# Optimization experiments

Hardware: AMD Instinct MI355X
Metric: run time of the kernel (lower is better)

The kernel has to match this reference:

```python
import jax, jax.numpy as jnp
import numpy as np

NUM_HEADS = 16
WIN_H, WIN_W = 7, 7
DIM = 512
N = WIN_H * WIN_W  # 49 tokens per window
B_ = 2048          # num_windows * batch
NUM_WINDOWS = 64


def _relative_pos_indices(win_h, win_w):
    ch, cw = np.meshgrid(np.arange(win_h), np.arange(win_w), indexing='ij')
    coords = np.stack([ch, cw], axis=-1).reshape(-1, 2)          # (N, 2)
    rel = coords[None, :, :] - coords[:, None, :]                # (N, N, 2)
    rel[:, :, 0] += win_h - 1
    rel[:, :, 1] += win_w - 1
    rel[:, :, 0] *= 2 * win_w - 1
    return rel.sum(-1).reshape(-1).astype(np.int32)             # (N*N,)


def setup_inputs() -> dict:
    key = jax.random.key(0)
    k1, k2, k3, k4, k5 = jax.random.split(key, 5)
    x = jax.random.normal(k1, (B_, N, DIM), dtype=jnp.float32)
    # 0 / -100 shift mask (finite stand-in for -inf; same softmax effect)
    u = jax.random.uniform(k2, (NUM_WINDOWS, N, N))
    mask = jnp.where(u < 0.2, -100.0, 0.0).astype(jnp.float32)
    qkv_w = jax.random.normal(k3, (DIM, 3 * DIM), dtype=jnp.float32) * 0.02
    qkv_b = jnp.zeros((3 * DIM,), jnp.float32)
    proj_w = jax.random.normal(k4, (DIM, DIM), dtype=jnp.float32) * 0.02
    proj_b = jnp.zeros((DIM,), jnp.float32)
    bias_table = jax.random.normal(k5, ((2 * WIN_H - 1) * (2 * WIN_W - 1), NUM_HEADS), dtype=jnp.float32) * 0.02
    rel_idx = jnp.asarray(_relative_pos_indices(WIN_H, WIN_W))
    return {"x": x, "mask": mask, "qkv_w": qkv_w, "qkv_b": qkv_b,
            "proj_w": proj_w, "proj_b": proj_b,
            "bias_table": bias_table, "rel_idx": rel_idx}


def reference(x, mask, qkv_w, qkv_b, proj_w, proj_b, bias_table, rel_idx):
    b_, n, c = x.shape
    h = NUM_HEADS
    d = c // h
    scale = d ** -0.5
    qkv = (x @ qkv_w + qkv_b).reshape(b_, n, 3, h, d)
    q, k, v = jnp.moveaxis(qkv, 2, 0)                 # each (b_, n, h, d)
    attn = jnp.einsum('bnhd,bmhd->bhnm', q * scale, k)  # (b_, h, n, n)
    # relative-position bias gather: (n*n,) -> (n, n, h) -> (h, n, n)
    bias = bias_table[rel_idx].reshape(n, n, h).transpose(2, 0, 1)
    attn = attn + bias[None]
    nw = mask.shape[0]
    attn = attn.reshape(b_ // nw, nw, h, n, n) + mask[None, :, None]
    attn = jax.nn.softmax(attn.reshape(b_, h, n, n), axis=-1)
    out = jnp.einsum('bhnm,bmhd->bnhd', attn, v).reshape(b_, n, c)
    return out @ proj_w + proj_b
```

## Files before the change

kernel.cpp:

```cpp
#include <hip/hip_runtime.h>
#include <stdint.h>

typedef __attribute__((ext_vector_type(8))) short short8;
typedef __attribute__((ext_vector_type(8))) unsigned short ushort8;
typedef __attribute__((ext_vector_type(4))) unsigned short bf16x4;
typedef __attribute__((ext_vector_type(4))) float float4_t;

#define AS1 __attribute__((address_space(1)))
#define AS3 __attribute__((address_space(3)))

__device__ __forceinline__ unsigned short f2bf(float f) {
    union { float f; unsigned u; } c; c.f = f;
    return (unsigned short)((c.u + 0x7fffu + ((c.u >> 16) & 1u)) >> 16);
}

__device__ __forceinline__ void load16_lds(const void* g, void* l) {
    __builtin_amdgcn_global_load_lds((const AS1 void*)(uintptr_t)g,
                                     (AS3 void*)(uintptr_t)l, 16, 0, 0);
}

__global__ __launch_bounds__(256)
void cvt_x(const float4_t* __restrict__ x, unsigned short* __restrict__ xb, int n8) {
    int i = blockIdx.x * 256 + threadIdx.x;
    if (i >= n8) return;
    float4_t a = x[2 * i], b = x[2 * i + 1];
    ushort8 v;
    v[0] = f2bf(a[0]); v[1] = f2bf(a[1]); v[2] = f2bf(a[2]); v[3] = f2bf(a[3]);
    v[4] = f2bf(b[0]); v[5] = f2bf(b[1]); v[6] = f2bf(b[2]); v[7] = f2bf(b[3]);
    ((ushort8*)xb)[i] = v;
}

__global__ __launch_bounds__(256)
void prep(const float* __restrict__ qkv_w, const float* __restrict__ proj_w,
          const float* __restrict__ bias_tab, const int* __restrict__ rel_idx,
          const float* __restrict__ mask,
          unsigned short* __restrict__ qkv_wT, unsigned short* __restrict__ proj_wT,
          float* __restrict__ biasP, float* __restrict__ maskP) {
    int i = blockIdx.x * 256 + threadIdx.x;
    if (i < 786432) {
        int n = i >> 9, k = i & 511;
        qkv_wT[i] = f2bf(qkv_w[k * 1536 + n]);
    } else if (i < 1048576) {
        int j = i - 786432;
        int n = j >> 9, k = j & 511;
        proj_wT[j] = f2bf(proj_w[k * 512 + n]);
    } else if (i < 1098752) {
        int j = i - 1048576;
        int h = j / 3136, mn = j % 3136;
        int m = mn >> 6, n = mn & 63;
        biasP[j] = (n < 49) ? bias_tab[rel_idx[m * 49 + n] * 16 + h] : 0.0f;
    } else {
        int j = i - 1098752;
        int w = j / 3136, mn = j % 3136;
        int m = mn >> 6, n = mn & 63;
        maskP[j] = (n < 49) ? mask[w * 2401 + m * 49 + n] : -1e30f;
    }
}

template <int MODE>
__global__ __launch_bounds__(256)
void gemm_bt(const unsigned short* __restrict__ A, const unsigned short* __restrict__ B,
             void* __restrict__ Cv, const float* __restrict__ bias,
             int M, int N, int K, float qscale) {
    __shared__ __align__(16) unsigned short As[4 * 128 * 32];
    __shared__ __align__(16) unsigned short Bs[4 * 128 * 32];

    const int t = threadIdx.x;
    const int lane = t & 63;
    const int wave = t >> 6;
    const int col = lane & 15;
    const int quad = lane >> 4;
    const int wm = (wave & 1) * 64;
    const int wn = (wave >> 1) * 64;

    const int nwg = gridDim.x;
    const int cpx = nwg >> 3;
    const int wg = (blockIdx.x & 7) * cpx + (blockIdx.x >> 3);
    const int nbx = N >> 7;
    const int m0 = (wg / nbx) * 128;
    const int n0 = (wg % nbx) * 128;

    float4_t acc[4][4] = {};

    const int row = t >> 2;
    const int seg = t & 3;
    const unsigned short* Ag0 = A + (size_t)(m0 + row) * K + seg * 8;
    const unsigned short* Ag1 = A + (size_t)(m0 + 64 + row) * K + seg * 8;
    const unsigned short* Bg0 = B + (size_t)(n0 + row) * K + seg * 8;
    const unsigned short* Bg1 = B + (size_t)(n0 + 64 + row) * K + seg * 8;

    auto stage = [&](int tile) {
        const int kk = tile << 5;
        unsigned short* Ad = As + ((tile & 3) << 12);
        unsigned short* Bd = Bs + ((tile & 3) << 12);
        load16_lds(Ag0 + kk, Ad + t * 8);
        load16_lds(Ag1 + kk, Ad + 2048 + t * 8);
        load16_lds(Bg0 + kk, Bd + t * 8);
        load16_lds(Bg1 + kk, Bd + 2048 + t * 8);
    };

    const int nt = K >> 5;
    stage(0); stage(1); stage(2);

    for (int tt = 0; tt < nt; ++tt) {
        if (tt < nt - 2)       asm volatile("s_waitcnt vmcnt(8)" ::: "memory");
        else if (tt == nt - 2) asm volatile("s_waitcnt vmcnt(4)" ::: "memory");
        else                   asm volatile("s_waitcnt vmcnt(0)" ::: "memory");
        __builtin_amdgcn_s_barrier();
        asm volatile("" ::: "memory");

        if (tt + 3 < nt) stage(tt + 3);

        const unsigned short* Ab = As + ((size_t)(tt & 3) << 12);
        const unsigned short* Bb = Bs + ((size_t)(tt & 3) << 12);
        short8 a[4], b[4];
#pragma unroll
        for (int i = 0; i < 4; ++i)
            a[i] = *(const short8*)&Ab[(wm + i * 16 + col) * 32 + quad * 8];
#pragma unroll
        for (int j = 0; j < 4; ++j)
            b[j] = *(const short8*)&Bb[(wn + j * 16 + col) * 32 + quad * 8];
        __builtin_amdgcn_s_setprio(1);
#pragma unroll
        for (int i = 0; i < 4; ++i)
#pragma unroll
            for (int j = 0; j < 4; ++j)
                acc[i][j] = __builtin_amdgcn_mfma_f32_16x16x32_bf16(b[j], a[i], acc[i][j], 0, 0, 0);
        __builtin_amdgcn_s_setprio(0);
    }

    if (MODE == 0) {
        unsigned short* C = (unsigned short*)Cv;
#pragma unroll
        for (int j = 0; j < 4; ++j) {
            int gc0 = n0 + wn + j * 16 + quad * 4;
            float4_t bv = *(const float4_t*)&bias[gc0];
            float sc = (gc0 < 512) ? qscale : 1.0f;
#pragma unroll
            for (int i = 0; i < 4; ++i) {
                int gr = m0 + wm + i * 16 + col;
                bf16x4 u;
#pragma unroll
                for (int r = 0; r < 4; ++r) u[r] = f2bf((acc[i][j][r] + bv[r]) * sc);
                *(bf16x4*)&C[(size_t)gr * N + gc0] = u;
            }
        }
    } else {
        float* C = (float*)Cv;
#pragma unroll
        for (int j = 0; j < 4; ++j) {
            int gc0 = n0 + wn + j * 16 + quad * 4;
            float4_t bv = *(const float4_t*)&bias[gc0];
#pragma unroll
            for (int i = 0; i < 4; ++i) {
                int gr = m0 + wm + i * 16 + col;
                float4_t ov = acc[i][j] + bv;
                *(float4_t*)&C[(size_t)gr * N + gc0] = ov;
            }
        }
    }
}

__global__ __launch_bounds__(64)
void attn_win(const unsigned short* __restrict__ qkv,
              const float* __restrict__ maskP,
              const float* __restrict__ biasP,
              unsigned short* __restrict__ attn_out) {
    __shared__ __align__(16) unsigned short P[64 * 64];
    __shared__ __align__(16) unsigned short Vt[32 * 64];

    const int bh = blockIdx.x;
    const int w = bh >> 4;
    const int hh = bh & 15;
    const int lane = threadIdx.x;
    const int col = lane & 15;
    const int quad = lane >> 4;
    const size_t rowbase = (size_t)(w * 49) * 1536;

    {
        ushort8 u0 = {}, u1 = {}, u2 = {}, u3 = {};
        if (lane < 49) {
            const ushort8* vp = (const ushort8*)(qkv + rowbase + (size_t)lane * 1536 + 1024 + hh * 32);
            u0 = vp[0]; u1 = vp[1]; u2 = vp[2]; u3 = vp[3];
        }
#pragma unroll
        for (int c = 0; c < 8; ++c) {
            Vt[((c) * 64 + lane) ^ ((c & 7) << 3)] = u0[c];
            Vt[((c + 8) * 64 + lane) ^ ((c & 7) << 3)] = u1[c];
            Vt[((c + 16) * 64 + lane) ^ ((c & 7) << 3)] = u2[c];
            Vt[((c + 24) * 64 + lane) ^ ((c & 7) << 3)] = u3[c];
        }
    }

    float4_t s[4][4] = {};
    {
        short8 qf[4], kf[4];
#pragma unroll
        for (int i = 0; i < 4; ++i) {
            int m = i * 16 + col; if (m > 48) m = 48;
            qf[i] = *(const short8*)(qkv + rowbase + (size_t)m * 1536 + hh * 32 + quad * 8);
            kf[i] = *(const short8*)(qkv + rowbase + (size_t)m * 1536 + 512 + hh * 32 + quad * 8);
        }
        __builtin_amdgcn_s_setprio(1);
#pragma unroll
        for (int i = 0; i < 4; ++i)
#pragma unroll
            for (int j = 0; j < 4; ++j)
                s[i][j] = __builtin_amdgcn_mfma_f32_16x16x32_bf16(kf[j], qf[i], s[i][j], 0, 0, 0);
        __builtin_amdgcn_s_setprio(0);
    }

    {
        const float* mk = maskP + (size_t)(w & 63) * 3136;
        const float* bs = biasP + (size_t)hh * 3136;
#pragma unroll
        for (int i = 0; i < 4; ++i) {
            int mc = i * 16 + col; if (mc > 48) mc = 48;
#pragma unroll
            for (int j = 0; j < 4; ++j) {
                int n0 = j * 16 + quad * 4;
                float4_t a4 = *(const float4_t*)&mk[mc * 64 + n0];
                float4_t b4 = *(const float4_t*)&bs[mc * 64 + n0];
#pragma unroll
                for (int r = 0; r < 4; ++r) s[i][j][r] += a4[r] + b4[r];
            }
        }
    }

#pragma unroll
    for (int i = 0; i < 4; ++i) {
        int m = i * 16 + col;
        float mx = s[i][0][0];
#pragma unroll
        for (int j = 0; j < 4; ++j)
#pragma unroll
            for (int r = 0; r < 4; ++r) mx = fmaxf(mx, s[i][j][r]);
        mx = fmaxf(mx, __shfl_xor(mx, 16));
        mx = fmaxf(mx, __shfl_xor(mx, 32));
        float sum = 0.f;
#pragma unroll
        for (int j = 0; j < 4; ++j)
#pragma unroll
            for (int r = 0; r < 4; ++r) {
                float e = __expf(s[i][j][r] - mx);
                s[i][j][r] = e; sum += e;
            }
        sum += __shfl_xor(sum, 16);
        sum += __shfl_xor(sum, 32);
        float inv = 1.0f / sum;
#pragma unroll
        for (int j = 0; j < 4; ++j) {
            bf16x4 u;
#pragma unroll
            for (int r = 0; r < 4; ++r) u[r] = f2bf(s[i][j][r] * inv);
            *(bf16x4*)&P[(m * 64 + j * 16 + quad * 4) ^ ((m & 7) << 3)] = u;
        }
    }
    __syncthreads();

    float4_t o[4][2] = {};
#pragma unroll
    for (int s2 = 0; s2 < 2; ++s2) {
        short8 pa[4], vb[2];
#pragma unroll
        for (int i = 0; i < 4; ++i) {
            int m = i * 16 + col;
            pa[i] = *(const short8*)&P[(m * 64 + s2 * 32 + quad * 8) ^ ((m & 7) << 3)];
        }
#pragma unroll
        for (int tj = 0; tj < 2; ++tj) {
            int d = tj * 16 + col;
            vb[tj] = *(const short8*)&Vt[(d * 64 + s2 * 32 + quad * 8) ^ ((d & 7) << 3)];
        }
        __builtin_amdgcn_s_setprio(1);
#pragma unroll
        for (int i = 0; i < 4; ++i)
#pragma unroll
            for (int tj = 0; tj < 2; ++tj)
                o[i][tj] = __builtin_amdgcn_mfma_f32_16x16x32_bf16(vb[tj], pa[i], o[i][tj], 0, 0, 0);
        __builtin_amdgcn_s_setprio(0);
    }

#pragma unroll
    for (int i = 0; i < 4; ++i) {
        int m = i * 16 + col;
        if (m < 49) {
            size_t ob = (size_t)(w * 49 + m) * 512 + hh * 32 + quad * 4;
#pragma unroll
            for (int tj = 0; tj < 2; ++tj) {
                bf16x4 u;
#pragma unroll
                for (int r = 0; r < 4; ++r) u[r] = f2bf(o[i][tj][r]);
                *(bf16x4*)&attn_out[ob + tj * 16] = u;
            }
        }
    }
}

extern "C" void kernel_launch(void* const* d_in, const int* in_sizes, int n_in,
                              void* d_out, int out_size, void* d_ws, size_t ws_size,
                              hipStream_t stream) {
    const float* x        = (const float*)d_in[0];
    const float* mask     = (const float*)d_in[1];
    const float* qkv_w    = (const float*)d_in[2];
    const float* qkv_b    = (const float*)d_in[3];
    const float* proj_w   = (const float*)d_in[4];
    const float* proj_b   = (const float*)d_in[5];
    const float* bias_tab = (const float*)d_in[6];
    const int*   rel_idx  = (const int*)d_in[7];
    float* out = (float*)d_out;

    char* ws = (char*)d_ws;
    size_t off = 0;
    auto carve = [&](size_t bytes) -> char* {
        char* p = ws + off;
        off += (bytes + 255) & ~(size_t)255;
        return p;
    };
    unsigned short* x_bf    = (unsigned short*)carve((size_t)51380224 * 2);
    unsigned short* qkv_wT  = (unsigned short*)carve((size_t)786432 * 2);
    unsigned short* proj_wT = (unsigned short*)carve((size_t)262144 * 2);
    float*          biasP   = (float*)carve((size_t)50176 * 4);
    float*          maskP   = (float*)carve((size_t)200704 * 4);
    unsigned short* qkv_o   = (unsigned short*)carve((size_t)100352 * 1536 * 2);
    unsigned short* attn_o  = x_bf;

    cvt_x<<<25088, 256, 0, stream>>>((const float4_t*)x, x_bf, 6422528);
    prep<<<5076, 256, 0, stream>>>(qkv_w, proj_w, bias_tab, rel_idx, mask,
                                   qkv_wT, proj_wT, biasP, maskP);
    gemm_bt<0><<<9408, 256, 0, stream>>>(x_bf, qkv_wT, (void*)qkv_o, qkv_b,
                                         100352, 1536, 512, 0.17677669529663687f);
    attn_win<<<32768, 64, 0, stream>>>(qkv_o, maskP, biasP, attn_o);
    gemm_bt<1><<<3136, 256, 0, stream>>>(attn_o, proj_wT, (void*)out, proj_b,
                                         100352, 512, 512, 1.0f);
}
```

Before: 916.7 us.

## Enlarge GEMM tiles to 256x256 with 8 waves and split-phase pipelined staging

The bf16 GEMM moves from 128x128 tiles with 4 waves to 256x256 tiles with 8 waves. Each wave now computes a 128x64 sub-tile in two halves. A and B staging into LDS is interleaved with the two MFMA halves, with more barriers and a reworked vmcnt wait schedule, so that loads overlap compute and more data is reused from LDS. The cost is doubled LDS (128KB per block), higher register pressure from 32 accumulators per lane, and fewer blocks, which can reduce occupancy and add tail effects.

```diff
diff --git a/kernel.cpp b/kernel.cpp
--- a/kernel.cpp
+++ b/kernel.cpp
@@ -58,103 +58,125 @@
 }
 
 template <int MODE>
-__global__ __launch_bounds__(256)
+__global__ __launch_bounds__(512, 2)
 void gemm_bt(const unsigned short* __restrict__ A, const unsigned short* __restrict__ B,
              void* __restrict__ Cv, const float* __restrict__ bias,
              int M, int N, int K, float qscale) {
-    __shared__ __align__(16) unsigned short As[4 * 128 * 32];
-    __shared__ __align__(16) unsigned short Bs[4 * 128 * 32];
+    __shared__ __align__(16) unsigned short As[4 * 256 * 32];
+    __shared__ __align__(16) unsigned short Bs[4 * 256 * 32];
 
     const int t = threadIdx.x;
     const int lane = t & 63;
     const int wave = t >> 6;
     const int col = lane & 15;
     const int quad = lane >> 4;
-    const int wm = (wave & 1) * 64;
-    const int wn = (wave >> 1) * 64;
+    const int wm = (wave >> 2) * 128;
+    const int wn = (wave & 3) * 64;
 
     const int nwg = gridDim.x;
     const int cpx = nwg >> 3;
     const int wg = (blockIdx.x & 7) * cpx + (blockIdx.x >> 3);
-    const int nbx = N >> 7;
-    const int m0 = (wg / nbx) * 128;
-    const int n0 = (wg % nbx) * 128;
-
-    float4_t acc[4][4] = {};
-
-    const int row = t >> 2;
-    const int seg = t & 3;
-    const unsigned short* Ag0 = A + (size_t)(m0 + row) * K + seg * 8;
-    const unsigned short* Ag1 = A + (size_t)(m0 + 64 + row) * K + seg * 8;
-    const unsigned short* Bg0 = B + (size_t)(n0 + row) * K + seg * 8;
-    const unsigned short* Bg1 = B + (size_t)(n0 + 64 + row) * K + seg * 8;
-
-    auto stage = [&](int tile) {
+    const int nbx = N >> 8;
+    const int m0 = (wg / nbx) * 256;
+    const int n0 = (wg % nbx) * 256;
+
+    float4_t acc[8][4] = {};
+
+    const int srow = t >> 2;
+    const int sseg = t & 3;
+    const unsigned short* Ag = A + (size_t)(m0 + srow) * K + sseg * 8;
+    const unsigned short* Bg = B + (size_t)(n0 + srow) * K + sseg * 8;
+    const size_t rstep = (size_t)128 * K;
+
+    auto stageA = [&](int tile) {
         const int kk = tile << 5;
-        unsigned short* Ad = As + ((tile & 3) << 12);
-        unsigned short* Bd = Bs + ((tile & 3) << 12);
-        load16_lds(Ag0 + kk, Ad + t * 8);
-        load16_lds(Ag1 + kk, Ad + 2048 + t * 8);
-        load16_lds(Bg0 + kk, Bd + t * 8);
-        load16_lds(Bg1 + kk, Bd + 2048 + t * 8);
+        unsigned short* d = As + ((tile & 3) << 13);
+        load16_lds(Ag + kk, d + t * 8);
+        load16_lds(Ag + rstep + kk, d + 4096 + t * 8);
     };
+    auto stageB = [&](int tile) {
+        const int kk = tile << 5;
+        unsigned short* d = Bs + ((tile & 3) << 13);
+        load16_lds(Bg + kk, d + t * 8);
+        load16_lds(Bg + rstep + kk, d + 4096 + t * 8);
+    };
 
     const int nt = K >> 5;
-    stage(0); stage(1); stage(2);
+    stageA(0); stageB(0); stageA(1); stageB(1); stageA(2); stageB(2);
+    asm volatile("s_waitcnt vmcnt(8)" ::: "memory");
+    __builtin_amdgcn_s_barrier();
+    asm volatile("" ::: "memory");
 
     for (int tt = 0; tt < nt; ++tt) {
-        if (tt < nt - 2)       asm volatile("s_waitcnt vmcnt(8)" ::: "memory");
-        else if (tt == nt - 2) asm volatile("s_waitcnt vmcnt(4)" ::: "memory");
-        else                   asm volatile("s_waitcnt vmcnt(0)" ::: "memory");
+        const unsigned short* Ab = As + ((tt & 3) << 13);
+        const unsigned short* Bb = Bs + ((tt & 3) << 13);
+
+        short8 b[4], a[4];
+#pragma unroll
+        for (int nf = 0; nf < 4; ++nf)
+            b[nf] = *(const short8*)&Bb[(wn + nf * 16 + col) * 32 + quad * 8];
+#pragma unroll
+        for (int mf = 0; mf < 4; ++mf)
+            a[mf] = *(const short8*)&Ab[(wm + mf * 16 + col) * 32 + quad * 8];
+        if (tt + 3 < nt) stageA(tt + 3);
         __builtin_amdgcn_s_barrier();
         asm volatile("" ::: "memory");
-
-        if (tt + 3 < nt) stage(tt + 3);
-
-        const unsigned short* Ab = As + ((size_t)(tt & 3) << 12);
-        const unsigned short* Bb = Bs + ((size_t)(tt & 3) << 12);
-        short8 a[4], b[4];
-#pragma unroll
-        for (int i = 0; i < 4; ++i)
-            a[i] = *(const short8*)&Ab[(wm + i * 16 + col) * 32 + quad * 8];
-#pragma unroll
-        for (int j = 0; j < 4; ++j)
-            b[j] = *(const short8*)&Bb[(wn + j * 16 + col) * 32 + quad * 8];
         __builtin_amdgcn_s_setprio(1);
 #pragma unroll
-        for (int i = 0; i < 4; ++i)
-#pragma unroll
-            for (int j = 0; j < 4; ++j)
-                acc[i][j] = __builtin_amdgcn_mfma_f32_16x16x32_bf16(b[j], a[i], acc[i][j], 0, 0, 0);
+        for (int mf = 0; mf < 4; ++mf)
+#pragma unroll
+            for (int nf = 0; nf < 4; ++nf)
+                acc[mf][nf] = __builtin_amdgcn_mfma_f32_16x16x32_bf16(b[nf], a[mf], acc[mf][nf], 0, 0, 0);
         __builtin_amdgcn_s_setprio(0);
+        __builtin_amdgcn_s_barrier();
+        asm volatile("" ::: "memory");
+
+#pragma unroll
+        for (int mf = 0; mf < 4; ++mf)
+            a[mf] = *(const short8*)&Ab[(wm + 64 + mf * 16 + col) * 32 + quad * 8];
+        if (tt + 3 < nt) stageB(tt + 3);
+        if (tt < nt - 3)       asm volatile("s_waitcnt vmcnt(8)" ::: "memory");
+        else if (tt == nt - 3) asm volatile("s_waitcnt vmcnt(4)" ::: "memory");
+        else if (tt == nt - 2) asm volatile("s_waitcnt vmcnt(0)" ::: "memory");
+        __builtin_amdgcn_s_barrier();
+        asm volatile("" ::: "memory");
+        __builtin_amdgcn_s_setprio(1);
+#pragma unroll
+        for (int mf = 0; mf < 4; ++mf)
+#pragma unroll
+            for (int nf = 0; nf < 4; ++nf)
+                acc[4 + mf][nf] = __builtin_amdgcn_mfma_f32_16x16x32_bf16(b[nf], a[mf], acc[4 + mf][nf], 0, 0, 0);
+        __builtin_amdgcn_s_setprio(0);
+        __builtin_amdgcn_s_barrier();
+        asm volatile("" ::: "memory");
     }
 
     if (MODE == 0) {
         unsigned short* C = (unsigned short*)Cv;
 #pragma unroll
-        for (int j = 0; j < 4; ++j) {
-            int gc0 = n0 + wn + j * 16 + quad * 4;
+        for (int nf = 0; nf < 4; ++nf) {
+            int gc0 = n0 + wn + nf * 16 + quad * 4;
             float4_t bv = *(const float4_t*)&bias[gc0];
             float sc = (gc0 < 512) ? qscale : 1.0f;
 #pragma unroll
-            for (int i = 0; i < 4; ++i) {
-                int gr = m0 + wm + i * 16 + col;
+            for (int mf = 0; mf < 8; ++mf) {
+                int gr = m0 + wm + mf * 16 + col;
                 bf16x4 u;
 #pragma unroll
-                for (int r = 0; r < 4; ++r) u[r] = f2bf((acc[i][j][r] + bv[r]) * sc);
+                for (int r = 0; r < 4; ++r) u[r] = f2bf((acc[mf][nf][r] + bv[r]) * sc);
                 *(bf16x4*)&C[(size_t)gr * N + gc0] = u;
             }
         }
     } else {
         float* C = (float*)Cv;
 #pragma unroll
-        for (int j = 0; j < 4; ++j) {
-            int gc0 = n0 + wn + j * 16 + quad * 4;
+        for (int nf = 0; nf < 4; ++nf) {
+            int gc0 = n0 + wn + nf * 16 + quad * 4;
             float4_t bv = *(const float4_t*)&bias[gc0];
 #pragma unroll
-            for (int i = 0; i < 4; ++i) {
-                int gr = m0 + wm + i * 16 + col;
-                float4_t ov = acc[i][j] + bv;
+            for (int mf = 0; mf < 8; ++mf) {
+                int gr = m0 + wm + mf * 16 + col;
+                float4_t ov = acc[mf][nf] + bv;
                 *(float4_t*)&C[(size_t)gr * N + gc0] = ov;
             }
         }
@@ -328,9 +350,9 @@
     cvt_x<<<25088, 256, 0, stream>>>((const float4_t*)x, x_bf, 6422528);
     prep<<<5076, 256, 0, stream>>>(qkv_w, proj_w, bias_tab, rel_idx, mask,
                                    qkv_wT, proj_wT, biasP, maskP);
-    gemm_bt<0><<<9408, 256, 0, stream>>>(x_bf, qkv_wT, (void*)qkv_o, qkv_b,
+    gemm_bt<0><<<2352, 512, 0, stream>>>(x_bf, qkv_wT, (void*)qkv_o, qkv_b,
                                          100352, 1536, 512, 0.17677669529663687f);
     attn_win<<<32768, 64, 0, stream>>>(qkv_o, maskP, biasP, attn_o);
-    gemm_bt<1><<<3136, 256, 0, stream>>>(attn_o, proj_wT, (void*)out, proj_b,
-                                         100352, 512, 512, 1.0f);
-}
+    gemm_bt<1><<<784, 512, 0, stream>>>(attn_o, proj_wT, (void*)out, proj_b,
+                                        100352, 512, 512, 1.0f);
+}
```

Measured after the change: 929.4 us. No clear change (+1.4%).
